# Kernel optimization log

Hardware: AMD Instinct MI355X
Metric: run time of the kernel (lower is better)

Reference implementation:

```python
import jax, jax.numpy as jnp
import numpy as np

B, T, D, H = 8, 4096, 1024, 64


def setup_inputs() -> dict:
    key = jax.random.key(0)
    ks = jax.random.split(key, 16)
    s = 0.02
    return {
        "x": jax.random.normal(ks[0], (B, T, D), jnp.float32),
        "norm_w": jnp.ones((D,), jnp.float32),
        "W1": jax.random.normal(ks[1], (D, D), jnp.float32) * s,
        "W2": jax.random.normal(ks[2], (D, D), jnp.float32) * s,
        "Wlast": jax.random.normal(ks[3], (D, D), jnp.float32) * s,
        "conv_w": jax.random.normal(ks[4], (D, 3), jnp.float32) * s,  # depthwise k=3, tap 0 = oldest
        "conv_b": jnp.zeros((D,), jnp.float32),
        "A": jnp.log(jnp.arange(1, H + 1, dtype=jnp.float32)),
        "Bw": jax.random.normal(ks[5], (H, D), jnp.float32) * s,
        "Bb": jnp.zeros((H,), jnp.float32),
        "Cw": jax.random.normal(ks[6], (D, H), jnp.float32) * s,
        "Cb": jnp.zeros((D,), jnp.float32),
        "Dw": jax.random.normal(ks[7], (D, D), jnp.float32) * s,
        "Db": jnp.zeros((D,), jnp.float32),
        "dw": jax.random.normal(ks[8], (H, D), jnp.float32) * s,
        "db": jnp.zeros((H,), jnp.float32),
    }


def reference(x, norm_w, W1, W2, Wlast, conv_w, conv_b, A, Bw, Bb, Cw, Cb, Dw, Db, dw, db):
    eps = jnp.finfo(x.dtype).eps  # torch RMSNorm default eps
    res = x
    xn = x * jax.lax.rsqrt(jnp.mean(x * x, axis=-1, keepdims=True) + eps) * norm_w
    x_b = xn @ W1.T
    z = xn @ W2.T
    # causal depthwise conv, kernel_size=3, left-pad 2
    xp = jnp.pad(x_b, ((0, 0), (2, 0), (0, 0)))
    xc = xp[:, :-2] * conv_w[:, 0] + xp[:, 1:-1] * conv_w[:, 1] + xp[:, 2:] * conv_w[:, 2] + conv_b
    xc = jax.nn.silu(xc)
    # log-space selective scan (cumprod(exp(A)) == exp(cumsum(A)))
    delta = jax.nn.softplus(xc @ dw.T + db)          # (B,T,H)
    A_log = -jax.nn.softplus(A)                      # (H,)
    A_bar_log = delta * A_log
    B_bar = delta * (xc @ Bw.T + Bb)
    A_cum = jnp.clip(jnp.cumsum(A_bar_log, axis=1), -20.0, 20.0)
    A_shift = jnp.concatenate([jnp.zeros_like(A_cum[:, :1]), A_cum[:, :-1]], axis=1)
    h = jnp.exp(A_cum) * jnp.cumsum(B_bar * jnp.exp(-A_shift), axis=1)
    y = h @ Cw.T + Cb + (xc @ Dw.T + Db)
    out = (y * jax.nn.silu(z)) @ Wlast.T + res
    return out
```

## Files before the change

kernel.cpp:

```cpp
#include <hip/hip_runtime.h>
#include <stdint.h>
#include <stddef.h>

#define TDIM 4096
#define DDIM 1024
#define HDIM 64
#define BDIM 8
#define MROWS (BDIM * TDIM)
#define KCAT (DDIM + HDIM)
#define DD (DDIM * DDIM)
#define HD (HDIM * DDIM)

typedef unsigned short ushort_t;
typedef __attribute__((ext_vector_type(8))) short short8;
typedef __attribute__((ext_vector_type(4))) float floatx4;

__device__ __forceinline__ unsigned short f2bf(float f) {
  unsigned u = __float_as_uint(f);
  u += 0x7fffu + ((u >> 16) & 1u);
  return (unsigned short)(u >> 16);
}
__device__ __forceinline__ float bf2f(unsigned short s) {
  return __uint_as_float(((unsigned)s) << 16);
}
__device__ __forceinline__ float softplusf(float x) {
  return x > 20.f ? x : log1pf(expf(x));
}

__global__ void k_prep(const float* __restrict__ W1, const float* __restrict__ W2,
                       const float* __restrict__ Wlast, const float* __restrict__ dwm,
                       const float* __restrict__ Bw, const float* __restrict__ Dw,
                       const float* __restrict__ Cw, const float* __restrict__ Cb,
                       const float* __restrict__ Db,
                       ushort_t* __restrict__ wcat, ushort_t* __restrict__ wlb,
                       ushort_t* __restrict__ dwbw, ushort_t* __restrict__ bcat,
                       float* __restrict__ biasCD) {
  int i = blockIdx.x * 256 + threadIdx.x;
  if (i < DD) { wcat[i] = f2bf(W1[i]); return; }
  i -= DD;
  if (i < DD) { wcat[DD + i] = f2bf(W2[i]); return; }
  i -= DD;
  if (i < DD) { wlb[i] = f2bf(Wlast[i]); return; }
  i -= DD;
  if (i < HD) { dwbw[i] = f2bf(dwm[i]); return; }
  i -= HD;
  if (i < HD) { dwbw[HD + i] = f2bf(Bw[i]); return; }
  i -= HD;
  if (i < DDIM * KCAT) {
    const int row = i / KCAT, k = i - row * KCAT;
    const float v = (k < DDIM) ? Dw[row * DDIM + k] : Cw[row * HDIM + (k - DDIM)];
    bcat[i] = f2bf(v);
    return;
  }
  i -= DDIM * KCAT;
  if (i < DDIM) biasCD[i] = Cb[i] + Db[i];
}

__global__ __launch_bounds__(256) void k_rms(const float* __restrict__ x,
                                             const float* __restrict__ nw,
                                             ushort_t* __restrict__ xn) {
  const int row = blockIdx.x;
  const int tid = threadIdx.x;
  const size_t base = (size_t)row * DDIM + tid * 4;
  const float4 xv = *(const float4*)(x + base);
  float ss = xv.x * xv.x + xv.y * xv.y + xv.z * xv.z + xv.w * xv.w;
  for (int off = 32; off > 0; off >>= 1) ss += __shfl_down(ss, off, 64);
  __shared__ float sws[4];
  const int lane = tid & 63, w = tid >> 6;
  if (lane == 0) sws[w] = ss;
  __syncthreads();
  const float tot = sws[0] + sws[1] + sws[2] + sws[3];
  const float scale = rsqrtf(tot * (1.0f / DDIM) + 1.1920929e-7f);
  const float4 nwv = *(const float4*)(nw + tid * 4);
  ushort4 o;
  o.x = f2bf(xv.x * scale * nwv.x);
  o.y = f2bf(xv.y * scale * nwv.y);
  o.z = f2bf(xv.z * scale * nwv.z);
  o.w = f2bf(xv.w * scale * nwv.w);
  *(ushort4*)(xn + base) = o;
}

__global__ __launch_bounds__(256) void k_conv(const ushort_t* __restrict__ xz,
                                              const float* __restrict__ cw,
                                              const float* __restrict__ cb,
                                              ushort_t* __restrict__ acat) {
  const size_t eidx = ((size_t)blockIdx.x * 256 + threadIdx.x) * 8;
  const int d = (int)(eidx & (DDIM - 1));
  const size_t m = eidx >> 10;
  const int t = (int)(m & (TDIM - 1));
  const size_t s = m * 2048 + d;
  const short8 r2 = *(const short8*)(xz + s);
  short8 r1 = {0,0,0,0,0,0,0,0}, r0 = {0,0,0,0,0,0,0,0};
  if (t >= 1) r1 = *(const short8*)(xz + s - 2048);
  if (t >= 2) r0 = *(const short8*)(xz + s - 4096);
  short8 o;
#pragma unroll
  for (int e = 0; e < 8; ++e) {
    const int de = d + e;
    float v = bf2f((ushort_t)r2[e]) * cw[de * 3 + 2]
            + bf2f((ushort_t)r1[e]) * cw[de * 3 + 1]
            + bf2f((ushort_t)r0[e]) * cw[de * 3 + 0]
            + cb[de];
    o[e] = (short)f2bf(v / (1.f + __expf(-v)));
  }
  *(short8*)(acat + m * KCAT + d) = o;
}

__global__ __launch_bounds__(256) void k_scan(const float* __restrict__ preG,
                                              const float* __restrict__ db,
                                              const float* __restrict__ Bb,
                                              const float* __restrict__ A,
                                              ushort_t* __restrict__ hT) {
  const int ch = blockIdx.x;
  const int b = ch >> 6, h = ch & 63;
  const int tid = threadIdx.x;
  const float dbh = db[h], Bbh = Bb[h];
  const float al = -softplusf(A[h]);
  const size_t base1 = (size_t)h * MROWS + (size_t)b * TDIM + (size_t)tid * 16;
  const size_t base2 = base1 + (size_t)64 * MROWS;

  float a[16], bbv[16];
#pragma unroll
  for (int k4 = 0; k4 < 4; ++k4) {
    const float4 p1 = *(const float4*)(preG + base1 + k4 * 4);
    const float4 p2 = *(const float4*)(preG + base2 + k4 * 4);
    const float pp1[4] = {p1.x, p1.y, p1.z, p1.w};
    const float pp2[4] = {p2.x, p2.y, p2.z, p2.w};
#pragma unroll
    for (int e = 0; e < 4; ++e) {
      const float delta = softplusf(pp1[e] + dbh);
      a[k4 * 4 + e] = delta * al;
      bbv[k4 * 4 + e] = delta * (pp2[e] + Bbh);
    }
  }
  float run = 0.f;
#pragma unroll
  for (int k = 0; k < 16; ++k) { run += a[k]; a[k] = run; }

  __shared__ float sh[256];
  sh[tid] = run;
  __syncthreads();
  for (int s = 1; s < 256; s <<= 1) {
    float v = (tid >= s) ? sh[tid - s] : 0.f;
    __syncthreads();
    sh[tid] += v;
    __syncthreads();
  }
  const float off = (tid > 0) ? sh[tid - 1] : 0.f;
  __syncthreads();

  float term[16];
  float prev = off;
#pragma unroll
  for (int k = 0; k < 16; ++k) {
    const float Pk = off + a[k];
    const float Ashift = fminf(fmaxf(prev, -20.f), 20.f);
    term[k] = bbv[k] * expf(-Ashift);
    a[k] = fminf(fmaxf(Pk, -20.f), 20.f);
    prev = Pk;
  }

  float run2 = 0.f;
#pragma unroll
  for (int k = 0; k < 16; ++k) { run2 += term[k]; term[k] = run2; }
  sh[tid] = run2;
  __syncthreads();
  for (int s = 1; s < 256; s <<= 1) {
    float v = (tid >= s) ? sh[tid - s] : 0.f;
    __syncthreads();
    sh[tid] += v;
    __syncthreads();
  }
  const float off2 = (tid > 0) ? sh[tid - 1] : 0.f;

  ushort_t* dst = hT + (size_t)h * MROWS + (size_t)b * TDIM + (size_t)tid * 16;
#pragma unroll
  for (int k = 0; k < 16; ++k) {
    dst[k] = f2bf(expf(a[k]) * (off2 + term[k]));
  }
}

__global__ __launch_bounds__(256) void k_htrans(const ushort_t* __restrict__ hT,
                                                ushort_t* __restrict__ acat) {
  __shared__ ushort_t t[64 * 256];
  const int tid = threadIdx.x;
  const int m0 = blockIdx.x * 256;
#pragma unroll
  for (int p = 0; p < 8; ++p) {
    const int e = p * 2048 + tid * 8;
    const int h = e >> 8, mm = e & 255;
    *(short8*)(t + e) = *(const short8*)(hT + (size_t)h * MROWS + m0 + mm);
  }
  __syncthreads();
  ushort_t* dst = acat + (size_t)(m0 + tid) * KCAT + DDIM;
#pragma unroll
  for (int p = 0; p < 8; ++p) {
    short8 v;
#pragma unroll
    for (int e = 0; e < 8; ++e) v[e] = t[(p * 8 + e) * 256 + tid];
    *(short8*)(dst + p * 8) = v;
  }
}

__device__ __forceinline__ void stage128x64(const ushort_t* __restrict__ G, int row0,
                                            int ld, int kc, ushort_t* s, int wave, int lane) {
  const int rsub = lane >> 3;
  const int cpos = lane & 7;
  using gp_t = const unsigned int __attribute__((address_space(1)))*;
  using lp_t = unsigned int __attribute__((address_space(3)))*;
#pragma unroll
  for (int g = 0; g < 4; ++g) {
    const int rg = wave * 4 + g;
    const int r = rg * 8 + rsub;
    const int c = cpos ^ rsub;
    const ushort_t* src = G + (size_t)(row0 + r) * (size_t)ld + (size_t)(kc + c * 8);
    __builtin_amdgcn_global_load_lds((gp_t)(const void*)src, (lp_t)(void*)(s + rg * 512),
                                     16, 0, 0);
  }
}

__global__ __launch_bounds__(256, 4) void k_gemm(
    const ushort_t* __restrict__ A, int lda,
    const ushort_t* __restrict__ Bt, int ldb,
    int nB, int Kdim, int mode,
    float* __restrict__ outF, ushort_t* __restrict__ outB, int ldc,
    const float* __restrict__ bias,
    const ushort_t* __restrict__ zmat, int ldz,
    const float* __restrict__ resid) {
  __shared__ alignas(16) ushort_t smem[128 * 128];
  ushort_t* sA = smem;
  ushort_t* sB = smem + 128 * 64;
  const int tid = threadIdx.x;
  const int wave = tid >> 6, lane = tid & 63;

  const int per = gridDim.x >> 3;
  const int xcd = blockIdx.x & 7, slot = blockIdx.x >> 3;
  const int tile = xcd * per + slot;
  const int m0 = (tile / nB) * 128, n0 = (tile % nB) * 128;

  const int half_m = (wave & 1) * 64, half_n = (wave >> 1) * 64;
  const int quad = lane >> 4, l16 = lane & 15;

  floatx4 acc[4][4];
#pragma unroll
  for (int i = 0; i < 4; ++i)
#pragma unroll
    for (int j = 0; j < 4; ++j) acc[i][j] = floatx4{0.f, 0.f, 0.f, 0.f};

  for (int kc = 0; kc < Kdim; kc += 64) {
    stage128x64(A, m0, lda, kc, sA, wave, lane);
    stage128x64(Bt, n0, ldb, kc, sB, wave, lane);
    __syncthreads();
#pragma unroll
    for (int s = 0; s < 2; ++s) {
      short8 af[4], bfr[4];
#pragma unroll
      for (int i = 0; i < 4; ++i) {
        const int r = half_m + i * 16 + l16;
        const int cp = (s * 4 + quad) ^ (r & 7);
        af[i] = *(const short8*)(sA + r * 64 + cp * 8);
      }
#pragma unroll
      for (int j = 0; j < 4; ++j) {
        const int r = half_n + j * 16 + l16;
        const int cp = (s * 4 + quad) ^ (r & 7);
        bfr[j] = *(const short8*)(sB + r * 64 + cp * 8);
      }
#pragma unroll
      for (int i = 0; i < 4; ++i)
#pragma unroll
        for (int j = 0; j < 4; ++j)
          acc[i][j] = __builtin_amdgcn_mfma_f32_16x16x32_bf16(af[i], bfr[j], acc[i][j], 0, 0, 0);
    }
    __syncthreads();
  }

#pragma unroll
  for (int i = 0; i < 4; ++i)
#pragma unroll
    for (int j = 0; j < 4; ++j)
#pragma unroll
      for (int rg = 0; rg < 4; ++rg) {
        const int r = half_m + i * 16 + quad * 4 + rg;
        const int c = half_n + j * 16 + l16;
        smem[r * 128 + c] = f2bf(acc[i][j][rg]);
      }
  __syncthreads();

#pragma unroll
  for (int p = 0; p < 8; ++p) {
    const int r = p * 16 + (tid >> 4);
    const int c = (tid & 15) * 8;
    short8 v8 = *(const short8*)(smem + r * 128 + c);
    const size_t m = (size_t)(m0 + r);
    const int n = n0 + c;
    if (mode == 0) {
      *(short8*)(outB + m * (size_t)ldc + n) = v8;
    } else if (mode == 1) {
      float* o = outF + m * (size_t)ldc + n;
#pragma unroll
      for (int e = 0; e < 8; ++e) o[e] = bf2f((ushort_t)v8[e]);
    } else if (mode == 2) {
      const short8 z8 = *(const short8*)(zmat + m * (size_t)ldz + n);
      short8 o;
#pragma unroll
      for (int e = 0; e < 8; ++e) {
        const float v = bf2f((ushort_t)v8[e]) + bias[n + e];
        const float zf = bf2f((ushort_t)z8[e]);
        o[e] = (short)f2bf(v * (zf / (1.f + __expf(-zf))));
      }
      *(short8*)(outB + m * (size_t)ldc + n) = o;
    } else {
      const float* rs = resid + m * (size_t)ldc + n;
      float* o = outF + m * (size_t)ldc + n;
#pragma unroll
      for (int e = 0; e < 8; ++e) o[e] = bf2f((ushort_t)v8[e]) + rs[e];
    }
  }
}

extern "C" void kernel_launch(void* const* d_in, const int* in_sizes, int n_in,
                              void* d_out, int out_size, void* d_ws, size_t ws_size,
                              hipStream_t stream) {
  const float* x      = (const float*)d_in[0];
  const float* norm_w = (const float*)d_in[1];
  const float* W1     = (const float*)d_in[2];
  const float* W2     = (const float*)d_in[3];
  const float* Wlast  = (const float*)d_in[4];
  const float* conv_w = (const float*)d_in[5];
  const float* conv_b = (const float*)d_in[6];
  const float* Aarr   = (const float*)d_in[7];
  const float* Bw     = (const float*)d_in[8];
  const float* Bb     = (const float*)d_in[9];
  const float* Cw     = (const float*)d_in[10];
  const float* Cb     = (const float*)d_in[11];
  const float* Dw     = (const float*)d_in[12];
  const float* Db     = (const float*)d_in[13];
  const float* dwm    = (const float*)d_in[14];
  const float* dbv    = (const float*)d_in[15];

  char* ws = (char*)d_ws;
  ushort_t* xz   = (ushort_t*)(ws + 0);
  ushort_t* acat = (ushort_t*)(ws + 134217728);
  float*   preG  = (float*)(ws + 205520896);
  ushort_t* hT   = (ushort_t*)(ws + 222298112);
  ushort_t* xnu  = (ushort_t*)(ws + 226492416);
  ushort_t* wcat = (ushort_t*)(ws + 293601280);
  ushort_t* wlb  = (ushort_t*)(ws + 297795584);
  ushort_t* dwbw = (ushort_t*)(ws + 299892736);
  ushort_t* bcat = (ushort_t*)(ws + 300154880);
  float*  biasCD = (float*)(ws + 302383104);
  float*   outF  = (float*)d_out;

  {
    const int total = 3 * DD + 2 * HD + DDIM * KCAT + DDIM;
    k_prep<<<(total + 255) / 256, 256, 0, stream>>>(W1, W2, Wlast, dwm, Bw, Dw, Cw, Cb, Db,
                                                    wcat, wlb, dwbw, bcat, biasCD);
  }

  k_rms<<<MROWS, 256, 0, stream>>>(x, norm_w, xnu);

  k_gemm<<<256 * 16, 256, 0, stream>>>(xnu, DDIM, wcat, DDIM, 16, DDIM, 0,
                                       nullptr, xz, 2048, nullptr, nullptr, 0, nullptr);

  k_conv<<<(MROWS * DDIM) / (256 * 8), 256, 0, stream>>>(xz, conv_w, conv_b, acat);

  k_gemm<<<256, 256, 0, stream>>>(dwbw, DDIM, acat, KCAT, 256, DDIM, 1,
                                  preG, nullptr, MROWS, nullptr, nullptr, 0, nullptr);

  k_scan<<<BDIM * HDIM, 256, 0, stream>>>(preG, dbv, Bb, Aarr, hT);

  k_htrans<<<MROWS / 256, 256, 0, stream>>>(hT, acat);

  k_gemm<<<256 * 8, 256, 0, stream>>>(acat, KCAT, bcat, KCAT, 8, KCAT, 2,
                                      nullptr, xnu, DDIM, biasCD, xz + DDIM, 2048, nullptr);

  k_gemm<<<256 * 8, 256, 0, stream>>>(xnu, DDIM, wlb, DDIM, 8, DDIM, 3,
                                      outF, nullptr, DDIM, nullptr, nullptr, 0, x);

  (void)in_sizes; (void)n_in; (void)out_size; (void)ws_size;
}
```

Measured before the change: 687.3 us.

## Add 256x256-tile pipelined GEMM kernel for the three large projections

Adds a new 512-thread GEMM kernel with 256x256 output tiles that loads global memory straight into LDS through direct-to-LDS loads. It uses a swizzled LDS layout, double buffering and prefetch interleaved with MFMA phases, plus s_setprio and an XCD-aware tile mapping. It replaces the previous GEMM for the input projection, the C/D projection with gating, and the output projection. The larger tiles raise data reuse per tile and overlap loads with compute, at the cost of a 128 KB LDS footprint and heavy register pressure.

```diff
diff --git a/kernel.cpp b/kernel.cpp
--- a/kernel.cpp
+++ b/kernel.cpp
@@ -319,6 +319,200 @@
   }
 }
 
+template <int KIND>
+__device__ __forceinline__ void stage_unit(const ushort_t* __restrict__ G, int row0, int ld,
+                                           int kc, ushort_t* s, int wave, int lane) {
+  using gp_t = const unsigned int __attribute__((address_space(1)))*;
+  using lp_t = unsigned int __attribute__((address_space(3)))*;
+  const int rsub = lane >> 3;
+  const int cpos = lane & 7;
+#pragma unroll
+  for (int g = 0; g < 2; ++g) {
+    const int idx = wave * 2 + g;
+    int rg;
+    if (KIND == 0)      rg = idx + (idx >= 8 ? 8 : 0);
+    else if (KIND == 1) rg = idx + 8 + (idx >= 8 ? 8 : 0);
+    else if (KIND == 2) rg = idx;
+    else                rg = idx + 16;
+    const int r = rg * 8 + rsub;
+    const int c = cpos ^ rsub;
+    const ushort_t* src = G + (size_t)(row0 + r) * (size_t)ld + (size_t)(kc + c * 8);
+    __builtin_amdgcn_global_load_lds((gp_t)(const void*)src, (lp_t)(void*)(s + rg * 512),
+                                     16, 0, 0);
+  }
+}
+
+__device__ __forceinline__ short8 lds_frag(const ushort_t* s, int row, int chunk) {
+  return *(const short8*)(s + row * 64 + ((chunk ^ (row & 7)) * 8));
+}
+
+__global__ __launch_bounds__(512, 2) void k_gemm256(
+    const ushort_t* __restrict__ A, int lda,
+    const ushort_t* __restrict__ Bt, int ldb,
+    int nB, int Kdim, int mode,
+    float* __restrict__ outF, ushort_t* __restrict__ outB, int ldc,
+    const float* __restrict__ bias,
+    const ushort_t* __restrict__ zmat, int ldz,
+    const float* __restrict__ resid) {
+  __shared__ alignas(16) ushort_t smem[65536];
+  const int tid = threadIdx.x;
+  const int wave = tid >> 6, lane = tid & 63;
+  const int wm = wave >> 2, wn = wave & 3;
+  const int quad = lane >> 4, l16 = lane & 15;
+
+  const int per = gridDim.x >> 3;
+  const int xcd = blockIdx.x & 7, slot = blockIdx.x >> 3;
+  const int tile = xcd * per + slot;
+  const int m0 = (tile / nB) * 256, n0 = (tile % nB) * 256;
+  const int NT = Kdim >> 6;
+
+  floatx4 acc[8][4];
+#pragma unroll
+  for (int i = 0; i < 8; ++i)
+#pragma unroll
+    for (int j = 0; j < 4; ++j) acc[i][j] = floatx4{0.f, 0.f, 0.f, 0.f};
+
+  stage_unit<2>(Bt, n0, ldb, 0, smem + 16384, wave, lane);
+  stage_unit<3>(Bt, n0, ldb, 0, smem + 16384, wave, lane);
+  stage_unit<0>(A, m0, lda, 0, smem, wave, lane);
+  stage_unit<1>(A, m0, lda, 0, smem, wave, lane);
+  if (NT > 1) {
+    stage_unit<2>(Bt, n0, ldb, 64, smem + 32768 + 16384, wave, lane);
+    stage_unit<3>(Bt, n0, ldb, 64, smem + 32768 + 16384, wave, lane);
+    asm volatile("s_waitcnt vmcnt(4)");
+  } else {
+    asm volatile("s_waitcnt vmcnt(0)");
+  }
+  __builtin_amdgcn_s_barrier();
+
+  short8 af[2][4], bf[2][2][2];
+  const int rowA = wm * 128 + l16;
+  const int rowB = wn * 64 + l16;
+
+  for (int t = 0; t < NT; ++t) {
+    ushort_t* sAc = smem + (t & 1) * 32768;
+    ushort_t* sBc = sAc + 16384;
+    ushort_t* sAn = smem + ((t + 1) & 1) * 32768;
+    const int kc1 = (t + 1) << 6, kc2 = (t + 2) << 6;
+    const bool pA = (t + 1 < NT), pB = (t + 2 < NT);
+
+#pragma unroll
+    for (int kk = 0; kk < 2; ++kk) {
+#pragma unroll
+      for (int i = 0; i < 4; ++i) af[kk][i] = lds_frag(sAc, rowA + i * 16, kk * 4 + quad);
+#pragma unroll
+      for (int j = 0; j < 2; ++j) bf[0][kk][j] = lds_frag(sBc, rowB + j * 16, kk * 4 + quad);
+    }
+    if (pA) stage_unit<0>(A, m0, lda, kc1, sAn, wave, lane);
+    __builtin_amdgcn_s_barrier();
+    asm volatile("s_waitcnt lgkmcnt(0)");
+    __builtin_amdgcn_s_setprio(1);
+#pragma unroll
+    for (int kk = 0; kk < 2; ++kk)
+#pragma unroll
+      for (int i = 0; i < 4; ++i)
+#pragma unroll
+        for (int j = 0; j < 2; ++j)
+          acc[i][j] = __builtin_amdgcn_mfma_f32_16x16x32_bf16(af[kk][i], bf[0][kk][j], acc[i][j], 0, 0, 0);
+    __builtin_amdgcn_s_setprio(0);
+    __builtin_amdgcn_s_barrier();
+
+#pragma unroll
+    for (int kk = 0; kk < 2; ++kk)
+#pragma unroll
+      for (int j = 0; j < 2; ++j) bf[1][kk][j] = lds_frag(sBc, rowB + (2 + j) * 16, kk * 4 + quad);
+    if (pA) stage_unit<1>(A, m0, lda, kc1, sAn, wave, lane);
+    __builtin_amdgcn_s_barrier();
+    asm volatile("s_waitcnt lgkmcnt(0)");
+    __builtin_amdgcn_s_setprio(1);
+#pragma unroll
+    for (int kk = 0; kk < 2; ++kk)
+#pragma unroll
+      for (int i = 0; i < 4; ++i)
+#pragma unroll
+        for (int j = 0; j < 2; ++j)
+          acc[i][2 + j] = __builtin_amdgcn_mfma_f32_16x16x32_bf16(af[kk][i], bf[1][kk][j], acc[i][2 + j], 0, 0, 0);
+    __builtin_amdgcn_s_setprio(0);
+    __builtin_amdgcn_s_barrier();
+
+#pragma unroll
+    for (int kk = 0; kk < 2; ++kk)
+#pragma unroll
+      for (int i = 0; i < 4; ++i) af[kk][i] = lds_frag(sAc, rowA + 64 + i * 16, kk * 4 + quad);
+    if (pB) stage_unit<2>(Bt, n0, ldb, kc2, sBc, wave, lane);
+    __builtin_amdgcn_s_barrier();
+    asm volatile("s_waitcnt lgkmcnt(0)");
+    __builtin_amdgcn_s_setprio(1);
+#pragma unroll
+    for (int kk = 0; kk < 2; ++kk)
+#pragma unroll
+      for (int i = 0; i < 4; ++i)
+#pragma unroll
+        for (int j = 0; j < 2; ++j)
+          acc[4 + i][j] = __builtin_amdgcn_mfma_f32_16x16x32_bf16(af[kk][i], bf[0][kk][j], acc[4 + i][j], 0, 0, 0);
+    __builtin_amdgcn_s_setprio(0);
+    __builtin_amdgcn_s_barrier();
+
+    if (pB) stage_unit<3>(Bt, n0, ldb, kc2, sBc, wave, lane);
+    __builtin_amdgcn_s_barrier();
+    __builtin_amdgcn_s_setprio(1);
+#pragma unroll
+    for (int kk = 0; kk < 2; ++kk)
+#pragma unroll
+      for (int i = 0; i < 4; ++i)
+#pragma unroll
+        for (int j = 0; j < 2; ++j)
+          acc[4 + i][2 + j] = __builtin_amdgcn_mfma_f32_16x16x32_bf16(af[kk][i], bf[1][kk][j], acc[4 + i][2 + j], 0, 0, 0);
+    __builtin_amdgcn_s_setprio(0);
+    if (pB) asm volatile("s_waitcnt vmcnt(4)");
+    else    asm volatile("s_waitcnt vmcnt(0)");
+    __builtin_amdgcn_s_barrier();
+  }
+
+#pragma unroll
+  for (int i = 0; i < 8; ++i)
+#pragma unroll
+    for (int j = 0; j < 4; ++j)
+#pragma unroll
+      for (int rg = 0; rg < 4; ++rg) {
+        const int r = wm * 128 + i * 16 + quad * 4 + rg;
+        const int c = wn * 64 + j * 16 + l16;
+        smem[r * 256 + c] = f2bf(acc[i][j][rg]);
+      }
+  __syncthreads();
+
+#pragma unroll
+  for (int p = 0; p < 16; ++p) {
+    const int r = p * 16 + (tid >> 5);
+    const int c = (tid & 31) * 8;
+    short8 v8 = *(const short8*)(smem + r * 256 + c);
+    const size_t m = (size_t)(m0 + r);
+    const int n = n0 + c;
+    if (mode == 0) {
+      *(short8*)(outB + m * (size_t)ldc + n) = v8;
+    } else if (mode == 1) {
+      float* o = outF + m * (size_t)ldc + n;
+#pragma unroll
+      for (int e = 0; e < 8; ++e) o[e] = bf2f((ushort_t)v8[e]);
+    } else if (mode == 2) {
+      const short8 z8 = *(const short8*)(zmat + m * (size_t)ldz + n);
+      short8 o;
+#pragma unroll
+      for (int e = 0; e < 8; ++e) {
+        const float v = bf2f((ushort_t)v8[e]) + bias[n + e];
+        const float zf = bf2f((ushort_t)z8[e]);
+        o[e] = (short)f2bf(v * (zf / (1.f + __expf(-zf))));
+      }
+      *(short8*)(outB + m * (size_t)ldc + n) = o;
+    } else {
+      const float* rs = resid + m * (size_t)ldc + n;
+      float* o = outF + m * (size_t)ldc + n;
+#pragma unroll
+      for (int e = 0; e < 8; ++e) o[e] = bf2f((ushort_t)v8[e]) + rs[e];
+    }
+  }
+}
+
 extern "C" void kernel_launch(void* const* d_in, const int* in_sizes, int n_in,
                               void* d_out, int out_size, void* d_ws, size_t ws_size,
                               hipStream_t stream) {
@@ -360,8 +554,8 @@
 
   k_rms<<<MROWS, 256, 0, stream>>>(x, norm_w, xnu);
 
-  k_gemm<<<256 * 16, 256, 0, stream>>>(xnu, DDIM, wcat, DDIM, 16, DDIM, 0,
-                                       nullptr, xz, 2048, nullptr, nullptr, 0, nullptr);
+  k_gemm256<<<(MROWS / 256) * 8, 512, 0, stream>>>(xnu, DDIM, wcat, DDIM, 8, DDIM, 0,
+                                                   nullptr, xz, 2048, nullptr, nullptr, 0, nullptr);
 
   k_conv<<<(MROWS * DDIM) / (256 * 8), 256, 0, stream>>>(xz, conv_w, conv_b, acat);
 
@@ -372,11 +566,11 @@
 
   k_htrans<<<MROWS / 256, 256, 0, stream>>>(hT, acat);
 
-  k_gemm<<<256 * 8, 256, 0, stream>>>(acat, KCAT, bcat, KCAT, 8, KCAT, 2,
-                                      nullptr, xnu, DDIM, biasCD, xz + DDIM, 2048, nullptr);
-
-  k_gemm<<<256 * 8, 256, 0, stream>>>(xnu, DDIM, wlb, DDIM, 8, DDIM, 3,
-                                      outF, nullptr, DDIM, nullptr, nullptr, 0, x);
+  k_gemm256<<<(MROWS / 256) * 4, 512, 0, stream>>>(acat, KCAT, bcat, KCAT, 4, KCAT, 2,
+                                                   nullptr, xnu, DDIM, biasCD, xz + DDIM, 2048, nullptr);
+
+  k_gemm256<<<(MROWS / 256) * 4, 512, 0, stream>>>(xnu, DDIM, wlb, DDIM, 4, DDIM, 3,
+                                                   outF, nullptr, DDIM, nullptr, nullptr, 0, x);
 
   (void)in_sizes; (void)n_in; (void)out_size; (void)ws_size;
 }
```

Result: no change. 682.6 us (-0.7%).
